# Performance work log

Hardware: AMD Instinct MI355X
Metric: run time of the kernel (lower is better)

## Reference

```python
import jax, jax.numpy as jnp
import numpy as np

B_, T_, DIN, H, DZ, DX = 64, 256, 128, 256, 8, 8


def setup_inputs() -> dict:
    key = jax.random.key(0)
    ks = jax.random.split(key, 13)
    p = lambda k, sh: jax.random.normal(k, sh, dtype=jnp.float32) * 0.05
    return {
        "y": jax.random.normal(ks[0], (B_, T_, DIN), dtype=jnp.float32),
        "W_ih": p(ks[1], (3 * H, DIN)), "W_hh": p(ks[2], (3 * H, H)),
        "b_ih": p(ks[3], (3 * H,)), "b_hh": p(ks[4], (3 * H,)),
        "W_mz": p(ks[5], (DZ, H)), "b_mz": p(ks[6], (DZ,)),
        "W_mx": p(ks[7], (DX, H)), "b_mx": p(ks[8], (DX,)),
        "W_pz": p(ks[9], (2 * DZ, H)), "b_pz": p(ks[10], (2 * DZ,)),
        "W_cx": p(ks[11], (DX * DX, H)), "b_cx": p(ks[12], (DX * DX,)),
    }


def _gru(y, W_ih, W_hh, b_ih, b_hh):
    # torch nn.GRU (single layer, unidirectional, batch_first)
    B, T, _ = y.shape
    Hh = W_hh.shape[1]
    x_proj = jnp.einsum('btd,gd->btg', y, W_ih) + b_ih  # [B,T,3H]

    def step(h, xp):
        hp = h @ W_hh.T + b_hh
        xr, xz, xn = jnp.split(xp, 3, axis=-1)
        hr, hz, hn = jnp.split(hp, 3, axis=-1)
        r = jax.nn.sigmoid(xr + hr)
        z = jax.nn.sigmoid(xz + hz)
        n = jnp.tanh(xn + r * hn)
        h_new = (1.0 - z) * n + z * h
        return h_new, h_new

    h0 = jnp.zeros((B, Hh), dtype=y.dtype)
    _, hs = jax.lax.scan(step, h0, jnp.swapaxes(x_proj, 0, 1))
    return jnp.swapaxes(hs, 0, 1)  # [B,T,H]


def _forward(y, W_ih, W_hh, b_ih, b_hh, W_mz, b_mz, W_mx, b_mx, W_pz, b_pz, W_cx, b_cx):
    enc = _gru(y, W_ih, W_hh, b_ih, b_hh)                       # [B,T,H]
    mean_z = enc @ W_mz.T + b_mz                                 # [B,T,DZ]
    mean_x = enc @ W_mx.T + b_mx                                 # [B,T,DX]
    bd_z = enc @ W_pz.T + b_pz                                   # [B,T,2*DZ]  (apply_softplus=False)

    # banded cov: per latent dim, upper-bidiagonal cholesky factor [B,T,T]
    diag = jnp.moveaxis(jax.nn.softplus(bd_z[..., :DZ]), -1, 0)  # [DZ,B,T]
    off = jnp.moveaxis(bd_z[:, :-1, DZ:], -1, 0)                 # [DZ,B,T-1]
    B, T = diag.shape[1], diag.shape[2]
    idx = jnp.arange(T)
    chol_z = (jnp.zeros((DZ, B, T, T), dtype=y.dtype)
              .at[:, :, idx, idx].set(diag)
              .at[:, :, idx[:-1], idx[1:]].set(off))             # [DZ,B,T,T]

    # anchor first two x-dims at t=0 (in-place mutation in torch)
    mean_x = mean_x.at[:, :, :2].add(-mean_x[:, 0:1, :2])
    mean_x_flat = mean_x.reshape(B * T, DX)

    cov_x = enc @ W_cx.T + b_cx                                  # [B,T,DX*DX]
    cov_x_flat = cov_x.reshape(B * T, DX, DX)
    return mean_z, chol_z, mean_x_flat, cov_x_flat


def reference(y, W_ih, W_hh, b_ih, b_hh, W_mz, b_mz, W_mx, b_mx, W_pz, b_pz, W_cx, b_cx):
    return _forward(y, W_ih, W_hh, b_ih, b_hh, W_mz, b_mz, W_mx, b_mx, W_pz, b_pz, W_cx, b_cx)
```

## Files before the change

kernel.cpp:

```cpp
#include <hip/hip_runtime.h>
#include <cstdint>
#include <cstddef>

#define B_   64
#define T_   256
#define DIN_ 128
#define H_   256
#define G3_  768

__device__ __forceinline__ unsigned short f2h(float f) {
  _Float16 h = (_Float16)f;
  return __builtin_bit_cast(unsigned short, h);
}

__device__ __forceinline__ void dot2f(float& acc, unsigned a, unsigned b) {
  asm("v_dot2_f32_f16 %0, %1, %2, %0" : "+v"(acc) : "v"(a), "v"(b));
}

__global__ __launch_bounds__(256) void prep_kernel(
    const float* __restrict__ W_ih, const float* __restrict__ W_hh,
    const float* __restrict__ W_mz, const float* __restrict__ W_mx,
    const float* __restrict__ W_pz, const float* __restrict__ W_cx,
    float* __restrict__ WT_ih, float* __restrict__ WheadT,
    unsigned* __restrict__ Wreg) {
  int i = blockIdx.x * 256 + threadIdx.x;
  if (i < 98304) {
    int k = i / 768, g = i % 768;
    WT_ih[i] = W_ih[g * 128 + k];
  } else if (i < 98304 + 24576) {
    int j = i - 98304;
    int c = j >> 8, k = j & 255;
    float v;
    if (c < 8)       v = W_mz[c * 256 + k];
    else if (c < 16) v = W_mx[(c - 8) * 256 + k];
    else if (c < 32) v = W_pz[(c - 16) * 256 + k];
    else             v = W_cx[(c - 32) * 256 + k];
    WheadT[j] = v;
  } else {
    int m = i - 122880;
    int c = m & 3, n = m >> 2;
    int t = n & 511, j4 = n >> 9;
    int j = 4 * j4 + c;
    int a = j >> 5, qp = j & 31;
    int o = a * 128 + (t & 127);
    int k0 = ((t >> 7) << 6) + 2 * qp;
    unsigned short lo = f2h(W_hh[o * 256 + k0]);
    unsigned short hi = f2h(W_hh[o * 256 + k0 + 1]);
    Wreg[m] = ((unsigned)hi << 16) | (unsigned)lo;
  }
}

__global__ __launch_bounds__(256) void xproj_kernel(
    const float* __restrict__ y, const float* __restrict__ WT_ih,
    const float* __restrict__ b_ih, float* __restrict__ xp) {
  __shared__ float ylds[32][132];
  int tid = threadIdx.x;
  int row0 = blockIdx.x * 32;
  const float4* y4 = (const float4*)(y + (size_t)row0 * DIN_);
#pragma unroll
  for (int i = 0; i < 4; ++i) {
    int idx = i * 256 + tid;
    float4 v = y4[idx];
    int r = idx >> 5, c4 = (idx & 31) * 4;
    ylds[r][c4 + 0] = v.x; ylds[r][c4 + 1] = v.y;
    ylds[r][c4 + 2] = v.z; ylds[r][c4 + 3] = v.w;
  }
  __syncthreads();
  int tx = tid & 15, ty = tid >> 4;
  for (int c = 0; c < 6; ++c) {
    int col0 = c * 128 + tx * 8;
    float acc[2][8];
#pragma unroll
    for (int a = 0; a < 2; ++a)
#pragma unroll
      for (int b = 0; b < 8; ++b) acc[a][b] = 0.f;
#pragma unroll 4
    for (int k = 0; k < 128; ++k) {
      float4 w0 = *(const float4*)&WT_ih[k * 768 + col0];
      float4 w1 = *(const float4*)&WT_ih[k * 768 + col0 + 4];
      float a0 = ylds[ty * 2 + 0][k], a1 = ylds[ty * 2 + 1][k];
      acc[0][0] += a0 * w0.x; acc[0][1] += a0 * w0.y; acc[0][2] += a0 * w0.z; acc[0][3] += a0 * w0.w;
      acc[0][4] += a0 * w1.x; acc[0][5] += a0 * w1.y; acc[0][6] += a0 * w1.z; acc[0][7] += a0 * w1.w;
      acc[1][0] += a1 * w0.x; acc[1][1] += a1 * w0.y; acc[1][2] += a1 * w0.z; acc[1][3] += a1 * w0.w;
      acc[1][4] += a1 * w1.x; acc[1][5] += a1 * w1.y; acc[1][6] += a1 * w1.z; acc[1][7] += a1 * w1.w;
    }
    float4 b0 = *(const float4*)&b_ih[col0];
    float4 b1 = *(const float4*)&b_ih[col0 + 4];
#pragma unroll
    for (int a = 0; a < 2; ++a) {
      int row = row0 + ty * 2 + a;
      float4 o0, o1;
      o0.x = acc[a][0] + b0.x; o0.y = acc[a][1] + b0.y; o0.z = acc[a][2] + b0.z; o0.w = acc[a][3] + b0.w;
      o1.x = acc[a][4] + b1.x; o1.y = acc[a][5] + b1.y; o1.z = acc[a][6] + b1.z; o1.w = acc[a][7] + b1.w;
      *(float4*)&xp[(size_t)row * G3_ + col0] = o0;
      *(float4*)&xp[(size_t)row * G3_ + col0 + 4] = o1;
    }
  }
}

__global__ __launch_bounds__(512, 2) void gru_kernel(
    const float* __restrict__ xp, const unsigned* __restrict__ Wreg,
    const float* __restrict__ b_hh, float* __restrict__ enc) {
  int tid = threadIdx.x;
  int ks = tid >> 7;
  int og = tid & 127;
  int b = blockIdx.x;
  __shared__ alignas(16) unsigned short hsb[256];
  __shared__ alignas(16) float part[3104];
  unsigned w[192];
  const uint4* W4 = (const uint4*)Wreg;
#pragma unroll
  for (int j4 = 0; j4 < 48; ++j4) {
    uint4 q = W4[j4 * 512 + tid];
    w[4 * j4 + 0] = q.x; w[4 * j4 + 1] = q.y;
    w[4 * j4 + 2] = q.z; w[4 * j4 + 3] = q.w;
  }
  const float* xpb = xp + (size_t)b * (T_ * G3_);
  float* encb = enc + (size_t)b * (T_ * H_);
  float bhr = 0.f, bhz = 0.f, bhn = 0.f, hold = 0.f;
  float xr0 = 0.f, xz0 = 0.f, xn0 = 0.f, xr1 = 0.f, xz1 = 0.f, xn1 = 0.f;
  if (tid < 256) {
    bhr = b_hh[tid]; bhz = b_hh[256 + tid]; bhn = b_hh[512 + tid];
    xr0 = xpb[tid];        xz0 = xpb[256 + tid];        xn0 = xpb[512 + tid];
    xr1 = xpb[768 + tid];  xz1 = xpb[1024 + tid];       xn1 = xpb[1280 + tid];
    hsb[tid] = 0;
  }
  __syncthreads();
  for (int t = 0; t < T_; ++t) {
    float xr2 = 0.f, xz2 = 0.f, xn2 = 0.f;
    if (tid < 256) {
      int base = (t + 2) * G3_ + tid;
      xr2 = xpb[base]; xz2 = xpb[base + 256]; xn2 = xpb[base + 512];
    }
    float p0 = 0.f, p1 = 0.f, p2 = 0.f, p3 = 0.f, p4 = 0.f, p5 = 0.f;
    const uint4* hs = ((const uint4*)hsb) + (ks << 3);
#pragma unroll
    for (int r = 0; r < 8; ++r) {
      uint4 hq = hs[r];
      dot2f(p0, hq.x, w[(r << 2) + 0]);
      dot2f(p0, hq.y, w[(r << 2) + 1]);
      dot2f(p0, hq.z, w[(r << 2) + 2]);
      dot2f(p0, hq.w, w[(r << 2) + 3]);
      dot2f(p1, hq.x, w[32 + (r << 2) + 0]);
      dot2f(p1, hq.y, w[32 + (r << 2) + 1]);
      dot2f(p1, hq.z, w[32 + (r << 2) + 2]);
      dot2f(p1, hq.w, w[32 + (r << 2) + 3]);
      dot2f(p2, hq.x, w[64 + (r << 2) + 0]);
      dot2f(p2, hq.y, w[64 + (r << 2) + 1]);
      dot2f(p2, hq.z, w[64 + (r << 2) + 2]);
      dot2f(p2, hq.w, w[64 + (r << 2) + 3]);
      dot2f(p3, hq.x, w[96 + (r << 2) + 0]);
      dot2f(p3, hq.y, w[96 + (r << 2) + 1]);
      dot2f(p3, hq.z, w[96 + (r << 2) + 2]);
      dot2f(p3, hq.w, w[96 + (r << 2) + 3]);
      dot2f(p4, hq.x, w[128 + (r << 2) + 0]);
      dot2f(p4, hq.y, w[128 + (r << 2) + 1]);
      dot2f(p4, hq.z, w[128 + (r << 2) + 2]);
      dot2f(p4, hq.w, w[128 + (r << 2) + 3]);
      dot2f(p5, hq.x, w[160 + (r << 2) + 0]);
      dot2f(p5, hq.y, w[160 + (r << 2) + 1]);
      dot2f(p5, hq.z, w[160 + (r << 2) + 2]);
      dot2f(p5, hq.w, w[160 + (r << 2) + 3]);
    }
    int pb = ks * 776 + og;
    part[pb]       = p0;  part[pb + 128] = p1;
    part[pb + 256] = p2;  part[pb + 384] = p3;
    part[pb + 512] = p4;  part[pb + 640] = p5;
    __syncthreads();
    if (tid < 256) {
      int u = tid;
      float prer = bhr + ((part[u] + part[776 + u]) +
                          (part[1552 + u] + part[2328 + u]));
      float prez = bhz + ((part[256 + u] + part[1032 + u]) +
                          (part[1808 + u] + part[2584 + u]));
      float pren = bhn + ((part[512 + u] + part[1288 + u]) +
                          (part[2064 + u] + part[2840 + u]));
      float r_ = 1.f / (1.f + __expf(-(xr0 + prer)));
      float z_ = 1.f / (1.f + __expf(-(xz0 + prez)));
      float a = xn0 + r_ * pren;
      a = fminf(15.f, fmaxf(-15.f, a));
      float e = __expf(2.f * a);
      float n = (e - 1.f) / (e + 1.f);
      float hnew = (1.f - z_) * n + z_ * hold;
      hold = hnew;
      encb[t * H_ + u] = hnew;
      hsb[u] = f2h(hnew);
      xr0 = xr1; xz0 = xz1; xn0 = xn1;
      xr1 = xr2; xz1 = xz2; xn1 = xn2;
    }
    __syncthreads();
  }
}

__global__ void anchor_kernel(const float* __restrict__ enc,
                              const float* __restrict__ W_mx,
                              const float* __restrict__ b_mx,
                              float* __restrict__ anchor) {
  int tid = threadIdx.x;
  if (tid < 128) {
    int b = tid >> 1, d = tid & 1;
    const float* e = enc + (size_t)b * T_ * H_;
    float acc = b_mx[d];
    for (int k = 0; k < 256; ++k) acc += e[k] * W_mx[d * 256 + k];
    anchor[b * 2 + d] = acc;
  }
}

__global__ __launch_bounds__(384) void heads_kernel(
    const float* __restrict__ enc, const float* __restrict__ WheadT,
    const float* __restrict__ b_mz, const float* __restrict__ b_mx,
    const float* __restrict__ b_pz, const float* __restrict__ b_cx,
    const float* __restrict__ anchor,
    float* __restrict__ out_meanz, float* __restrict__ out_meanx,
    float* __restrict__ out_covx, float* __restrict__ stage) {
  __shared__ float el[32 * 256];
  int tid = threadIdx.x;
  int row0 = blockIdx.x * 32;
  const float4* e4 = (const float4*)(enc + (size_t)row0 * 256);
  float4* el4 = (float4*)el;
#pragma unroll
  for (int i = 0; i < 6; ++i) {
    int idx = i * 384 + tid;
    if (idx < 2048) el4[idx] = e4[idx];
  }
  __syncthreads();
  int rg = tid / 96, c = tid - rg * 96;
  const float4* Wc = (const float4*)(WheadT + c * 256);
  float acc[8];
#pragma unroll
  for (int r = 0; r < 8; ++r) acc[r] = 0.f;
  for (int k4 = 0; k4 < 64; ++k4) {
    float4 w4 = Wc[k4];
#pragma unroll
    for (int r = 0; r < 8; ++r) {
      float4 ev = el4[(rg * 8 + r) * 64 + k4];
      acc[r] += w4.x * ev.x; acc[r] += w4.y * ev.y;
      acc[r] += w4.z * ev.z; acc[r] += w4.w * ev.w;
    }
  }
#pragma unroll
  for (int r = 0; r < 8; ++r) {
    int row = row0 + rg * 8 + r;
    int bb = row >> 8;
    float a_ = acc[r];
    if (c < 8) {
      out_meanz[(size_t)row * 8 + c] = a_ + b_mz[c];
    } else if (c < 16) {
      int d = c - 8;
      float v = a_ + b_mx[d];
      if (d < 2) v -= anchor[bb * 2 + d];
      out_meanx[(size_t)row * 8 + d] = v;
    } else if (c < 32) {
      int d = c - 16;
      float v = a_ + b_pz[d];
      if (d < 8)
        v = (v > 0.f) ? (v + log1pf(__expf(-v))) : log1pf(__expf(v));
      stage[(size_t)row * 16 + d] = v;
    } else {
      int d = c - 32;
      out_covx[(size_t)row * 64 + d] = a_ + b_cx[d];
    }
  }
}

__global__ __launch_bounds__(256) void chol_kernel(
    const float* __restrict__ stage, float4* __restrict__ chol) {
  int i = blockIdx.x * 256 + threadIdx.x;
  int stride = gridDim.x * 256;
  for (; i < 8388608; i += stride) {
    int d = i >> 20;
    int bt = (i >> 6) & 16383;
    int t = bt & 255;
    int lane = i & 63;
    float vd = 0.f, vo = 0.f;
    if ((t >> 2) == lane)        vd = stage[bt * 16 + d];
    if (((t + 1) >> 2) == lane)  vo = stage[bt * 16 + 8 + d];
    int te = t & 3, oe = (t + 1) & 3;
    float4 v;
    v.x = (te == 0 ? vd : 0.f) + (oe == 0 ? vo : 0.f);
    v.y = (te == 1 ? vd : 0.f) + (oe == 1 ? vo : 0.f);
    v.z = (te == 2 ? vd : 0.f) + (oe == 2 ? vo : 0.f);
    v.w = (te == 3 ? vd : 0.f) + (oe == 3 ? vo : 0.f);
    chol[i] = v;
  }
}

extern "C" void kernel_launch(void* const* d_in, const int* in_sizes, int n_in,
                              void* d_out, int out_size, void* d_ws, size_t ws_size,
                              hipStream_t stream) {
  const float* y    = (const float*)d_in[0];
  const float* W_ih = (const float*)d_in[1];
  const float* W_hh = (const float*)d_in[2];
  const float* b_ih = (const float*)d_in[3];
  const float* b_hh = (const float*)d_in[4];
  const float* W_mz = (const float*)d_in[5];
  const float* b_mz = (const float*)d_in[6];
  const float* W_mx = (const float*)d_in[7];
  const float* b_mx = (const float*)d_in[8];
  const float* W_pz = (const float*)d_in[9];
  const float* b_pz = (const float*)d_in[10];
  const float* W_cx = (const float*)d_in[11];
  const float* b_cx = (const float*)d_in[12];

  float* out    = (float*)d_out;
  float* mean_z = out;
  float* chol   = out + 131072;
  float* mean_x = out + 33685504;
  float* cov_x  = out + 33816576;

  float* ws      = (float*)d_ws;
  float* WT_ih   = ws;
  float* WheadT  = ws + 98304;
  unsigned* Wreg = (unsigned*)(ws + 122880);
  float* anchor  = ws + 221184;
  float* stage   = ws + 221312;

  float* xp  = chol;
  float* enc = chol + 12582912;

  prep_kernel<<<864, 256, 0, stream>>>(W_ih, W_hh, W_mz, W_mx, W_pz, W_cx,
                                       WT_ih, WheadT, Wreg);
  xproj_kernel<<<512, 256, 0, stream>>>(y, WT_ih, b_ih, xp);
  gru_kernel<<<64, 512, 0, stream>>>(xp, Wreg, b_hh, enc);
  anchor_kernel<<<1, 128, 0, stream>>>(enc, W_mx, b_mx, anchor);
  heads_kernel<<<512, 384, 0, stream>>>(enc, WheadT, b_mz, b_mx, b_pz, b_cx,
                                        anchor, mean_z, mean_x, cov_x, stage);
  chol_kernel<<<8192, 256, 0, stream>>>(stage, (float4*)chol);
}
```

Baseline: 629.0 us.

## Split GRU recurrent weights between LDS and per-step global reloads; enlarge xproj tile

The GRU kernel no longer holds all 192 recurrent weight words per thread in registers. One third now lives in shared memory and the remaining two thirds are re-read from global memory (L2-resident) on every timestep. Register pressure drops, but each step now pays LDS and global load latency on the serial critical path. The xproj kernel also processes 64 rows per block instead of 32, giving each thread four output rows for more weight reuse at the cost of half as many blocks.

```diff
diff --git a/kernel.cpp b/kernel.cpp
--- a/kernel.cpp
+++ b/kernel.cpp
@@ -53,12 +53,12 @@
 __global__ __launch_bounds__(256) void xproj_kernel(
     const float* __restrict__ y, const float* __restrict__ WT_ih,
     const float* __restrict__ b_ih, float* __restrict__ xp) {
-  __shared__ float ylds[32][132];
+  __shared__ float ylds[64][132];
   int tid = threadIdx.x;
-  int row0 = blockIdx.x * 32;
+  int row0 = blockIdx.x * 64;
   const float4* y4 = (const float4*)(y + (size_t)row0 * DIN_);
 #pragma unroll
-  for (int i = 0; i < 4; ++i) {
+  for (int i = 0; i < 8; ++i) {
     int idx = i * 256 + tid;
     float4 v = y4[idx];
     int r = idx >> 5, c4 = (idx & 31) * 4;
@@ -69,26 +69,31 @@
   int tx = tid & 15, ty = tid >> 4;
   for (int c = 0; c < 6; ++c) {
     int col0 = c * 128 + tx * 8;
-    float acc[2][8];
-#pragma unroll
-    for (int a = 0; a < 2; ++a)
+    float acc[4][8];
+#pragma unroll
+    for (int a = 0; a < 4; ++a)
 #pragma unroll
       for (int b = 0; b < 8; ++b) acc[a][b] = 0.f;
 #pragma unroll 4
     for (int k = 0; k < 128; ++k) {
       float4 w0 = *(const float4*)&WT_ih[k * 768 + col0];
       float4 w1 = *(const float4*)&WT_ih[k * 768 + col0 + 4];
-      float a0 = ylds[ty * 2 + 0][k], a1 = ylds[ty * 2 + 1][k];
+      float a0 = ylds[ty * 4 + 0][k], a1 = ylds[ty * 4 + 1][k];
+      float a2 = ylds[ty * 4 + 2][k], a3 = ylds[ty * 4 + 3][k];
       acc[0][0] += a0 * w0.x; acc[0][1] += a0 * w0.y; acc[0][2] += a0 * w0.z; acc[0][3] += a0 * w0.w;
       acc[0][4] += a0 * w1.x; acc[0][5] += a0 * w1.y; acc[0][6] += a0 * w1.z; acc[0][7] += a0 * w1.w;
       acc[1][0] += a1 * w0.x; acc[1][1] += a1 * w0.y; acc[1][2] += a1 * w0.z; acc[1][3] += a1 * w0.w;
       acc[1][4] += a1 * w1.x; acc[1][5] += a1 * w1.y; acc[1][6] += a1 * w1.z; acc[1][7] += a1 * w1.w;
+      acc[2][0] += a2 * w0.x; acc[2][1] += a2 * w0.y; acc[2][2] += a2 * w0.z; acc[2][3] += a2 * w0.w;
+      acc[2][4] += a2 * w1.x; acc[2][5] += a2 * w1.y; acc[2][6] += a2 * w1.z; acc[2][7] += a2 * w1.w;
+      acc[3][0] += a3 * w0.x; acc[3][1] += a3 * w0.y; acc[3][2] += a3 * w0.z; acc[3][3] += a3 * w0.w;
+      acc[3][4] += a3 * w1.x; acc[3][5] += a3 * w1.y; acc[3][6] += a3 * w1.z; acc[3][7] += a3 * w1.w;
     }
     float4 b0 = *(const float4*)&b_ih[col0];
     float4 b1 = *(const float4*)&b_ih[col0 + 4];
 #pragma unroll
-    for (int a = 0; a < 2; ++a) {
-      int row = row0 + ty * 2 + a;
+    for (int a = 0; a < 4; ++a) {
+      int row = row0 + ty * 4 + a;
       float4 o0, o1;
       o0.x = acc[a][0] + b0.x; o0.y = acc[a][1] + b0.y; o0.z = acc[a][2] + b0.z; o0.w = acc[a][3] + b0.w;
       o1.x = acc[a][4] + b1.x; o1.y = acc[a][5] + b1.y; o1.z = acc[a][6] + b1.z; o1.w = acc[a][7] + b1.w;
@@ -98,23 +103,21 @@
   }
 }
 
-__global__ __launch_bounds__(512, 2) void gru_kernel(
+__global__ __launch_bounds__(512) __attribute__((amdgpu_waves_per_eu(2, 2)))
+void gru_kernel(
     const float* __restrict__ xp, const unsigned* __restrict__ Wreg,
     const float* __restrict__ b_hh, float* __restrict__ enc) {
   int tid = threadIdx.x;
   int ks = tid >> 7;
   int og = tid & 127;
   int b = blockIdx.x;
+  __shared__ alignas(16) uint4 wl[8192];
   __shared__ alignas(16) unsigned short hsb[256];
   __shared__ alignas(16) float part[3104];
-  unsigned w[192];
   const uint4* W4 = (const uint4*)Wreg;
 #pragma unroll
-  for (int j4 = 0; j4 < 48; ++j4) {
-    uint4 q = W4[j4 * 512 + tid];
-    w[4 * j4 + 0] = q.x; w[4 * j4 + 1] = q.y;
-    w[4 * j4 + 2] = q.z; w[4 * j4 + 3] = q.w;
-  }
+  for (int j4 = 0; j4 < 16; ++j4)
+    wl[j4 * 512 + tid] = W4[j4 * 512 + tid];
   const float* xpb = xp + (size_t)b * (T_ * G3_);
   float* encb = enc + (size_t)b * (T_ * H_);
   float bhr = 0.f, bhz = 0.f, bhn = 0.f, hold = 0.f;
@@ -127,40 +130,38 @@
   }
   __syncthreads();
   for (int t = 0; t < T_; ++t) {
+    uint4 s[32];
+#pragma unroll
+    for (int m = 0; m < 32; ++m) s[m] = W4[(16 + m) * 512 + tid];
     float xr2 = 0.f, xz2 = 0.f, xn2 = 0.f;
     if (tid < 256) {
       int base = (t + 2) * G3_ + tid;
       xr2 = xpb[base]; xz2 = xpb[base + 256]; xn2 = xpb[base + 512];
     }
+    const uint4* hs = ((const uint4*)hsb) + (ks << 3);
+    uint4 hq[8];
+#pragma unroll
+    for (int r = 0; r < 8; ++r) hq[r] = hs[r];
     float p0 = 0.f, p1 = 0.f, p2 = 0.f, p3 = 0.f, p4 = 0.f, p5 = 0.f;
-    const uint4* hs = ((const uint4*)hsb) + (ks << 3);
 #pragma unroll
     for (int r = 0; r < 8; ++r) {
-      uint4 hq = hs[r];
-      dot2f(p0, hq.x, w[(r << 2) + 0]);
-      dot2f(p0, hq.y, w[(r << 2) + 1]);
-      dot2f(p0, hq.z, w[(r << 2) + 2]);
-      dot2f(p0, hq.w, w[(r << 2) + 3]);
-      dot2f(p1, hq.x, w[32 + (r << 2) + 0]);
-      dot2f(p1, hq.y, w[32 + (r << 2) + 1]);
-      dot2f(p1, hq.z, w[32 + (r << 2) + 2]);
-      dot2f(p1, hq.w, w[32 + (r << 2) + 3]);
-      dot2f(p2, hq.x, w[64 + (r << 2) + 0]);
-      dot2f(p2, hq.y, w[64 + (r << 2) + 1]);
-      dot2f(p2, hq.z, w[64 + (r << 2) + 2]);
-      dot2f(p2, hq.w, w[64 + (r << 2) + 3]);
-      dot2f(p3, hq.x, w[96 + (r << 2) + 0]);
-      dot2f(p3, hq.y, w[96 + (r << 2) + 1]);
-      dot2f(p3, hq.z, w[96 + (r << 2) + 2]);
-      dot2f(p3, hq.w, w[96 + (r << 2) + 3]);
-      dot2f(p4, hq.x, w[128 + (r << 2) + 0]);
-      dot2f(p4, hq.y, w[128 + (r << 2) + 1]);
-      dot2f(p4, hq.z, w[128 + (r << 2) + 2]);
-      dot2f(p4, hq.w, w[128 + (r << 2) + 3]);
-      dot2f(p5, hq.x, w[160 + (r << 2) + 0]);
-      dot2f(p5, hq.y, w[160 + (r << 2) + 1]);
-      dot2f(p5, hq.z, w[160 + (r << 2) + 2]);
-      dot2f(p5, hq.w, w[160 + (r << 2) + 3]);
+      uint4 w0 = wl[r * 512 + tid];
+      uint4 w1 = wl[(8 + r) * 512 + tid];
+      dot2f(p0, hq[r].x, w0.x); dot2f(p0, hq[r].y, w0.y);
+      dot2f(p0, hq[r].z, w0.z); dot2f(p0, hq[r].w, w0.w);
+      dot2f(p1, hq[r].x, w1.x); dot2f(p1, hq[r].y, w1.y);
+      dot2f(p1, hq[r].z, w1.z); dot2f(p1, hq[r].w, w1.w);
+    }
+#pragma unroll
+    for (int r = 0; r < 8; ++r) {
+      dot2f(p2, hq[r].x, s[r].x);      dot2f(p2, hq[r].y, s[r].y);
+      dot2f(p2, hq[r].z, s[r].z);      dot2f(p2, hq[r].w, s[r].w);
+      dot2f(p3, hq[r].x, s[8 + r].x);  dot2f(p3, hq[r].y, s[8 + r].y);
+      dot2f(p3, hq[r].z, s[8 + r].z);  dot2f(p3, hq[r].w, s[8 + r].w);
+      dot2f(p4, hq[r].x, s[16 + r].x); dot2f(p4, hq[r].y, s[16 + r].y);
+      dot2f(p4, hq[r].z, s[16 + r].z); dot2f(p4, hq[r].w, s[16 + r].w);
+      dot2f(p5, hq[r].x, s[24 + r].x); dot2f(p5, hq[r].y, s[24 + r].y);
+      dot2f(p5, hq[r].z, s[24 + r].z); dot2f(p5, hq[r].w, s[24 + r].w);
     }
     int pb = ks * 776 + og;
     part[pb]       = p0;  part[pb + 128] = p1;
@@ -320,7 +321,7 @@
 
   prep_kernel<<<864, 256, 0, stream>>>(W_ih, W_hh, W_mz, W_mx, W_pz, W_cx,
                                        WT_ih, WheadT, Wreg);
-  xproj_kernel<<<512, 256, 0, stream>>>(y, WT_ih, b_ih, xp);
+  xproj_kernel<<<256, 256, 0, stream>>>(y, WT_ih, b_ih, xp);
   gru_kernel<<<64, 512, 0, stream>>>(xp, Wreg, b_hh, enc);
   anchor_kernel<<<1, 128, 0, stream>>>(enc, W_mx, b_mx, anchor);
   heads_kernel<<<512, 384, 0, stream>>>(enc, WheadT, b_mz, b_mx, b_pz, b_cx,
```

Measured after the change: 654.0 us. +4.0%, slower.
